# Kernel optimization log

Measured on AMD Instinct MI355X. Metric: run time of the kernel, lower is better.

Reference implementation:

```python
import jax, jax.numpy as jnp
import numpy as np

D_MODEL = 1024
HIDDEN = 4096
N_EXPERTS = 8
TOP_K = 2


def setup_inputs() -> dict:
    key = jax.random.key(0)
    ks = jax.random.split(key, 7)
    x = jax.random.normal(ks[0], (4, 2048, D_MODEL), dtype=jnp.float32)
    s = 0.02
    Wg = jax.random.normal(ks[1], (D_MODEL, N_EXPERTS), dtype=jnp.float32) * s
    bg = jnp.zeros((N_EXPERTS,), dtype=jnp.float32)
    W1 = jax.random.normal(ks[2], (N_EXPERTS, D_MODEL, HIDDEN), dtype=jnp.float32) * s
    b1 = jnp.zeros((N_EXPERTS, HIDDEN), dtype=jnp.float32)
    W2 = jax.random.normal(ks[3], (N_EXPERTS, HIDDEN, D_MODEL), dtype=jnp.float32) * s
    b2 = jnp.zeros((N_EXPERTS, D_MODEL), dtype=jnp.float32)
    return {"x": x, "Wg": Wg, "bg": bg, "W1": W1, "b1": b1, "W2": W2, "b2": b2}


def reference(x, Wg, bg, W1, b1, W2, b2):
    B, T, D = x.shape
    xf = x.reshape(-1, D)                      # (N, D)
    N = xf.shape[0]

    # --- top-k gate ---
    logits = xf @ Wg + bg                      # (N, E)
    all_probs = jax.nn.softmax(logits, axis=-1)
    topk_logits, topk_idx = jax.lax.top_k(logits, TOP_K)   # (N, k)
    topk_gates = jax.nn.softmax(topk_logits, axis=-1)      # (N, k), sums to 1

    # scatter gates into dense (N, E) masks (matches torch scatter_add_)
    rows = jnp.arange(N)[:, None]
    gate_mask = jnp.zeros((N, N_EXPERTS), dtype=xf.dtype).at[rows, topk_idx].add(topk_gates)
    dispatch_mask = jnp.zeros((N, N_EXPERTS), dtype=xf.dtype).at[rows, topk_idx].add(1.0)

    # --- experts: dense batched form; unselected tokens have gate 0 so math matches ---
    h = jnp.einsum('nd,edh->neh', xf, W1) + b1             # (N, E, H)
    h = jax.nn.relu(h)
    y = jnp.einsum('neh,ehd->ned', h, W2) + b2             # (N, E, D)
    out = jnp.einsum('ned,ne->nd', y, gate_mask)           # weighted combine
    outputs = out.reshape(B, T, D)

    # --- load-balance loss + metadata ---
    tokens_per_expert = (dispatch_mask > 0).sum(axis=0)
    assignment_fraction = gate_mask.sum(axis=0) / N
    expected_prob = all_probs.mean(axis=0)
    load_balance_loss = (expected_prob * assignment_fraction).sum() * N_EXPERTS

    return (outputs, load_balance_loss, tokens_per_expert, expected_prob, assignment_fraction)
```

## Files before the change

kernel.cpp:

```cpp
#include <hip/hip_runtime.h>
#include <stdint.h>

#define D_MODEL 1024
#define HID     4096
#define NE      8
#define NTOK    8192
#define NSLOT   (NTOK*2)
#define TM      128
#define MAX_RB  136
#define MPAD    (MAX_RB*TM)
#define HHALF   2048
#define GATE_BLOCKS 32

typedef unsigned short u16;
typedef __attribute__((ext_vector_type(8))) __bf16 bf16x8;
typedef __attribute__((ext_vector_type(4))) float  f32x4;

__device__ __forceinline__ u16 f2bu(float f){
  uint32_t u = __builtin_bit_cast(uint32_t, f);
  uint32_t r = (u + 0x7FFFu + ((u >> 16) & 1u)) >> 16;
  return (u16)r;
}

__device__ __forceinline__ void gload16(const u16* src, u16* lds){
  __builtin_amdgcn_global_load_lds((const __attribute__((address_space(1))) void*)src,
                                   (__attribute__((address_space(3))) void*)lds, 16, 0, 0);
}

__device__ __forceinline__ int xcd_swz(int w, int nwg){
  int q = nwg >> 3;
  return (w & 7) * q + (w >> 3);
}

#define WAITV(n) do{ asm volatile("s_waitcnt vmcnt(" #n ")" ::: "memory"); \
                     __builtin_amdgcn_sched_barrier(0); }while(0)
#define BARX()   do{ __builtin_amdgcn_sched_barrier(0); \
                     __builtin_amdgcn_s_barrier(); \
                     __builtin_amdgcn_sched_barrier(0); }while(0)

__global__ __launch_bounds__(256) void xcvt_kernel(const float* __restrict__ x, u16* __restrict__ x16){
  size_t i = (size_t)blockIdx.x*256 + threadIdx.x;
  const float4* p = (const float4*)(x + i*8);
  float4 a = p[0], b = p[1];
  u16 o[8] = {f2bu(a.x),f2bu(a.y),f2bu(a.z),f2bu(a.w),f2bu(b.x),f2bu(b.y),f2bu(b.z),f2bu(b.w)};
  *(int4*)(x16 + i*8) = *(int4*)o;
}

__global__ __launch_bounds__(256) void transpose_cvt(const float* __restrict__ in,
                                                     u16* __restrict__ out, int R, int C)
{
  __shared__ float tile[32][33];
  int e = blockIdx.z;
  int r0 = blockIdx.y * 32, c0 = blockIdx.x * 32;
  const float* src = in + (size_t)e * R * C;
  u16* dst = out + (size_t)e * R * C;
  int tx = threadIdx.x, ty = threadIdx.y;
#pragma unroll
  for (int i = 0; i < 4; i++){
    int r = r0 + ty + i*8;
    tile[ty + i*8][tx] = src[(size_t)r * C + c0 + tx];
  }
  __syncthreads();
#pragma unroll
  for (int i = 0; i < 4; i++){
    int c = c0 + ty + i*8;
    dst[(size_t)c * R + r0 + tx] = f2bu(tile[tx][ty + i*8]);
  }
}

__global__ __launch_bounds__(256) void gate_kernel(
    const float* __restrict__ x, const float* __restrict__ Wg, const float* __restrict__ bg,
    int* __restrict__ topk, float* __restrict__ gates,
    float* __restrict__ part_probs, float* __restrict__ part_assign, int* __restrict__ part_cnt)
{
  __shared__ float sp[256][8];
  __shared__ float sa[256][8];
  __shared__ int   sc[256][8];
  int t = threadIdx.x;
  int n = blockIdx.x * 256 + t;
  float lg[8];
#pragma unroll
  for (int e = 0; e < 8; e++) lg[e] = bg[e];
  const float4* xr = (const float4*)(x + (size_t)n * D_MODEL);
  for (int j = 0; j < D_MODEL/4; j++){
    float4 v = xr[j];
    const float* wr = Wg + (size_t)j * 32;
#pragma unroll
    for (int e = 0; e < 8; e++)
      lg[e] += v.x*wr[e] + v.y*wr[8+e] + v.z*wr[16+e] + v.w*wr[24+e];
  }
  float m = lg[0];
#pragma unroll
  for (int e = 1; e < 8; e++) m = fmaxf(m, lg[e]);
  float p[8]; float s = 0.f;
#pragma unroll
  for (int e = 0; e < 8; e++){ p[e] = expf(lg[e]-m); s += p[e]; }
  float inv = 1.f / s;
  int bi = 0; float best = lg[0];
#pragma unroll
  for (int e = 1; e < 8; e++) if (lg[e] > best){ best = lg[e]; bi = e; }
  int bi2 = 0; float best2 = -3.0e38f;
#pragma unroll
  for (int e = 0; e < 8; e++) if (e != bi && lg[e] > best2){ best2 = lg[e]; bi2 = e; }
  float t1 = expf(best2 - best);
  float g0 = 1.f / (1.f + t1);
  float g1 = t1 / (1.f + t1);
  topk[2*n] = bi;  topk[2*n+1] = bi2;
  gates[2*n] = g0; gates[2*n+1] = g1;
#pragma unroll
  for (int e = 0; e < 8; e++){
    sp[t][e] = p[e] * inv;
    sa[t][e] = (e == bi) ? g0 : ((e == bi2) ? g1 : 0.f);
    sc[t][e] = (e == bi || e == bi2) ? 1 : 0;
  }
  __syncthreads();
  if (t < 8){
    float s2 = 0.f; for (int i = 0; i < 256; i++) s2 += sp[i][t];
    part_probs[blockIdx.x*8 + t] = s2;
  } else if (t < 16){
    int e = t - 8; float s2 = 0.f; for (int i = 0; i < 256; i++) s2 += sa[i][e];
    part_assign[blockIdx.x*8 + e] = s2;
  } else if (t < 24){
    int e = t - 16; int c = 0; for (int i = 0; i < 256; i++) c += sc[i][e];
    part_cnt[blockIdx.x*8 + e] = c;
  }
}

__global__ __launch_bounds__(256) void scan_kernel(const int* __restrict__ part_cnt,
                                                   int* __restrict__ counts,
                                                   int* __restrict__ padded_off,
                                                   int* __restrict__ cursor,
                                                   int* __restrict__ block_expert,
                                                   int* __restrict__ routed)
{
  __shared__ int off[NE+1];
  int t = threadIdx.x;
  if (t == 0){
    int o = 0; off[0] = 0;
    for (int e = 0; e < NE; e++){
      int c = 0;
      for (int b = 0; b < GATE_BLOCKS; b++) c += part_cnt[b*8 + e];
      counts[e] = c;
      o += ((c + TM - 1) / TM) * TM;
      off[e+1] = o;
    }
    for (int e = 0; e <= NE; e++) padded_off[e] = off[e];
  }
  __syncthreads();
  if (t < NE) cursor[t] = 0;
  for (int rb = t; rb < MAX_RB; rb += 256){
    int e = -1;
    int r = rb * TM;
    for (int j = 0; j < NE; j++)
      if (r >= off[j] && r < off[j+1]) e = j;
    block_expert[rb] = e;
  }
  for (int i = t; i < MPAD; i += 256) routed[i] = -1;
}

__global__ __launch_bounds__(256) void place_kernel(const int* __restrict__ topk,
                                                    const int* __restrict__ padded_off,
                                                    int* __restrict__ cursor,
                                                    int* __restrict__ routed)
{
  int s = blockIdx.x * 256 + threadIdx.x;
  int e = topk[s];
  int pos = padded_off[e] + atomicAdd(&cursor[e], 1);
  routed[pos] = s;
}

__global__ __launch_bounds__(256, 3) void gemm1_kernel(
    const u16* __restrict__ x16, const u16* __restrict__ w1t, const float* __restrict__ b1,
    const int* __restrict__ routed, const int* __restrict__ block_expert,
    u16* __restrict__ h, int half)
{
  int l = xcd_swz(blockIdx.x, gridDim.x);
  int rb = l >> 4, cb = l & 15;
  int e = block_expert[rb];
  if (e < 0) return;
  __shared__ __align__(16) u16 Al[3][128][32];
  __shared__ __align__(16) u16 Bl[3][128][32];
  u16* AF = &Al[0][0][0];
  u16* BF = &Bl[0][0][0];
  int t = threadIdx.x;
  int lane = t & 63, wid = t >> 6;

  int srow0 = wid*32 + (lane >> 2);
  int sch = ((lane & 3) ^ ((lane >> 3) & 3)) * 8;

  int slot0 = routed[rb*TM + srow0];
  int slot1 = routed[rb*TM + srow0 + 16];
  int tok0 = slot0 >= 0 ? (slot0 >> 1) : 0;
  int tok1 = slot1 >= 0 ? (slot1 >> 1) : 0;
  const u16* srcA0 = x16 + (size_t)tok0 * D_MODEL + sch;
  const u16* srcA1 = x16 + (size_t)tok1 * D_MODEL + sch;
  const u16* wb = w1t + ((size_t)e*HID + (size_t)half*HHALF + (size_t)cb*128) * D_MODEL + sch;
  const u16* srcB0 = wb + (size_t)srow0 * D_MODEL;
  const u16* srcB1 = wb + (size_t)(srow0 + 16) * D_MODEL;

  int wr = wid >> 1, wc = wid & 1;
  int fr = lane & 15, fk = lane >> 4;
  int fkx8 = (fk ^ ((fr >> 1) & 3)) * 8;
  f32x4 acc[4][4];
#pragma unroll
  for (int i = 0; i < 4; i++)
#pragma unroll
    for (int j = 0; j < 4; j++) acc[i][j] = (f32x4){0.f,0.f,0.f,0.f};

#define STG1(bo, kk) do{ \
    gload16(srcA0 + (kk), AF + (bo) + wid*1024); \
    gload16(srcA1 + (kk), AF + (bo) + wid*1024 + 512); \
    gload16(srcB0 + (kk), BF + (bo) + wid*1024); \
    gload16(srcB1 + (kk), BF + (bo) + wid*1024 + 512); } while(0)

#define CMP1(bo) do{ \
    bf16x8 af[4], bf[4]; \
    _Pragma("unroll") \
    for (int mm = 0; mm < 4; mm++) af[mm] = *(const bf16x8*)(AF + (bo) + (wr*64 + mm*16 + fr)*32 + fkx8); \
    _Pragma("unroll") \
    for (int nn = 0; nn < 4; nn++) bf[nn] = *(const bf16x8*)(BF + (bo) + (wc*64 + nn*16 + fr)*32 + fkx8); \
    _Pragma("unroll") \
    for (int mm = 0; mm < 4; mm++) \
      _Pragma("unroll") \
      for (int nn = 0; nn < 4; nn++) \
        acc[mm][nn] = __builtin_amdgcn_mfma_f32_16x16x32_bf16(af[mm], bf[nn], acc[mm][nn], 0, 0, 0); } while(0)

  const int nk = D_MODEL/32;
  STG1(0, 0); STG1(4096, 32); STG1(8192, 64);
  int bo = 0;
  for (int i = 0; i < nk - 2; i++){
    WAITV(8);
    BARX();
    CMP1(bo);
    BARX();
    if (i < nk - 3) STG1(bo, (i+3)*32);
    bo = (bo == 8192) ? 0 : bo + 4096;
  }
  WAITV(4); BARX(); CMP1(bo); BARX();
  bo = (bo == 8192) ? 0 : bo + 4096;
  WAITV(0); BARX(); CMP1(bo);

  int r4 = fk * 4;
#pragma unroll
  for (int nn = 0; nn < 4; nn++){
    int ct = wc*64 + nn*16 + fr;
    float bias = b1[(size_t)e*HID + (size_t)half*HHALF + cb*128 + ct];
#pragma unroll
    for (int mm = 0; mm < 4; mm++){
#pragma unroll
      for (int r = 0; r < 4; r++){
        int rt = wr*64 + mm*16 + r4 + r;
        float v = acc[mm][nn][r] + bias;
        v = v > 0.f ? v : 0.f;
        h[(size_t)(rb*TM + rt) * HHALF + cb*128 + ct] = f2bu(v);
      }
    }
  }
#undef STG1
#undef CMP1
}

__global__ __launch_bounds__(256, 3) void gemm2_kernel(
    const u16* __restrict__ h, const u16* __restrict__ w2t,
    const int* __restrict__ routed, const int* __restrict__ block_expert,
    const float* __restrict__ gates, float* __restrict__ y, int half)
{
  int l = xcd_swz(blockIdx.x, gridDim.x);
  int rb = l >> 3, cb = l & 7;
  int e = block_expert[rb];
  if (e < 0) return;
  __shared__ __align__(16) u16 Al[3][128][32];
  __shared__ __align__(16) u16 Bl[3][128][32];
  __shared__ int   rslot[128];
  __shared__ float rgate[128];
  u16* AF = &Al[0][0][0];
  u16* BF = &Bl[0][0][0];
  int t = threadIdx.x;
  int lane = t & 63, wid = t >> 6;
  if (t < 128){
    int s = routed[rb*TM + t];
    rslot[t] = s;
    rgate[t] = (s >= 0) ? gates[s] : 0.f;
  }

  int srow0 = wid*32 + (lane >> 2);
  int sch = ((lane & 3) ^ ((lane >> 3) & 3)) * 8;
  const u16* srcA0 = h + (size_t)(rb*TM + srow0) * HHALF + sch;
  const u16* srcA1 = h + (size_t)(rb*TM + srow0 + 16) * HHALF + sch;
  const u16* wb = w2t + ((size_t)e*D_MODEL + (size_t)cb*128) * HID + (size_t)half*HHALF + sch;
  const u16* srcB0 = wb + (size_t)srow0 * HID;
  const u16* srcB1 = wb + (size_t)(srow0 + 16) * HID;

  int wr = wid >> 1, wc = wid & 1;
  int fr = lane & 15, fk = lane >> 4;
  int fkx8 = (fk ^ ((fr >> 1) & 3)) * 8;
  f32x4 acc[4][4];
#pragma unroll
  for (int i = 0; i < 4; i++)
#pragma unroll
    for (int j = 0; j < 4; j++) acc[i][j] = (f32x4){0.f,0.f,0.f,0.f};

#define STG2(bo, kk) do{ \
    gload16(srcA0 + (kk), AF + (bo) + wid*1024); \
    gload16(srcA1 + (kk), AF + (bo) + wid*1024 + 512); \
    gload16(srcB0 + (kk), BF + (bo) + wid*1024); \
    gload16(srcB1 + (kk), BF + (bo) + wid*1024 + 512); } while(0)

#define CMP2(bo) do{ \
    bf16x8 af[4], bf[4]; \
    _Pragma("unroll") \
    for (int mm = 0; mm < 4; mm++) af[mm] = *(const bf16x8*)(AF + (bo) + (wr*64 + mm*16 + fr)*32 + fkx8); \
    _Pragma("unroll") \
    for (int nn = 0; nn < 4; nn++) bf[nn] = *(const bf16x8*)(BF + (bo) + (wc*64 + nn*16 + fr)*32 + fkx8); \
    _Pragma("unroll") \
    for (int mm = 0; mm < 4; mm++) \
      _Pragma("unroll") \
      for (int nn = 0; nn < 4; nn++) \
        acc[mm][nn] = __builtin_amdgcn_mfma_f32_16x16x32_bf16(af[mm], bf[nn], acc[mm][nn], 0, 0, 0); } while(0)

  const int nk = HHALF/32;
  STG2(0, 0); STG2(4096, 32); STG2(8192, 64);
  int bo = 0;
  for (int i = 0; i < nk - 2; i++){
    WAITV(8);
    BARX();
    CMP2(bo);
    BARX();
    if (i < nk - 3) STG2(bo, (i+3)*32);
    bo = (bo == 8192) ? 0 : bo + 4096;
  }
  WAITV(4); BARX(); CMP2(bo); BARX();
  bo = (bo == 8192) ? 0 : bo + 4096;
  WAITV(0); BARX(); CMP2(bo);

  int r4 = fk * 4;
#pragma unroll
  for (int mm = 0; mm < 4; mm++){
#pragma unroll
    for (int r = 0; r < 4; r++){
      int rt = wr*64 + mm*16 + r4 + r;
      int slot = rslot[rt];
      if (slot < 0) continue;
      float g = rgate[rt];
#pragma unroll
      for (int nn = 0; nn < 4; nn++){
        int ct = wc*64 + nn*16 + fr;
        size_t idx = (size_t)slot * D_MODEL + cb*128 + ct;
        float val = g * acc[mm][nn][r];
        if (half == 0) y[idx] = val;
        else           y[idx] += val;
      }
    }
  }
#undef STG2
#undef CMP2
}

__global__ __launch_bounds__(256) void combine_kernel(
    const float* __restrict__ y, const int* __restrict__ topk, const float* __restrict__ gates,
    const float* __restrict__ b2, float* __restrict__ out)
{
  int i = blockIdx.x * 256 + threadIdx.x;
  int n = i >> 8;
  int d = (i & 255) * 4;
  float4 a  = *(const float4*)(y + (size_t)(2*n)   * D_MODEL + d);
  float4 b  = *(const float4*)(y + (size_t)(2*n+1) * D_MODEL + d);
  int e0 = topk[2*n], e1 = topk[2*n+1];
  float g0 = gates[2*n], g1 = gates[2*n+1];
  float4 c0 = *(const float4*)(b2 + (size_t)e0 * D_MODEL + d);
  float4 c1 = *(const float4*)(b2 + (size_t)e1 * D_MODEL + d);
  float4 o;
  o.x = a.x + b.x + g0*c0.x + g1*c1.x;
  o.y = a.y + b.y + g0*c0.y + g1*c1.y;
  o.z = a.z + b.z + g0*c0.z + g1*c1.z;
  o.w = a.w + b.w + g0*c0.w + g1*c1.w;
  *(float4*)(out + (size_t)n * D_MODEL + d) = o;
}

__global__ void finalize_kernel(const float* __restrict__ part_probs,
                                const float* __restrict__ part_assign,
                                const int* __restrict__ counts,
                                float* __restrict__ out_tail)
{
  __shared__ float ep[8], af[8];
  int t = threadIdx.x;
  if (t < 8){
    float s = 0.f;
    for (int b = 0; b < GATE_BLOCKS; b++) s += part_probs[b*8 + t];
    ep[t] = s / (float)NTOK;
  } else if (t < 16){
    int e = t - 8; float s = 0.f;
    for (int b = 0; b < GATE_BLOCKS; b++) s += part_assign[b*8 + e];
    af[e] = s / (float)NTOK;
  }
  __syncthreads();
  if (t == 0){
    float loss = 0.f;
    for (int e = 0; e < 8; e++) loss += ep[e] * af[e];
    out_tail[0] = loss * (float)NE;
  }
  if (t < 8){
    out_tail[1 + t]  = (float)counts[t];
    out_tail[9 + t]  = ep[t];
    out_tail[17 + t] = af[t];
  }
}

extern "C" void kernel_launch(void* const* d_in, const int* in_sizes, int n_in,
                              void* d_out, int out_size, void* d_ws, size_t ws_size,
                              hipStream_t stream)
{
  const float* x  = (const float*)d_in[0];
  const float* Wg = (const float*)d_in[1];
  const float* bg = (const float*)d_in[2];
  const float* W1 = (const float*)d_in[3];
  const float* b1 = (const float*)d_in[4];
  const float* W2 = (const float*)d_in[5];
  const float* b2 = (const float*)d_in[6];
  float* out = (float*)d_out;

  char* ws = (char*)d_ws;
  size_t o = 0;
  auto alloc = [&](size_t bytes) -> char* {
    char* p = ws + o; o = (o + bytes + 255) & ~(size_t)255; return p;
  };
  int*   topk        = (int*)   alloc((size_t)NSLOT*4);
  float* gates       = (float*) alloc((size_t)NSLOT*4);
  int*   counts      = (int*)   alloc(NE*4);
  int*   padded_off  = (int*)   alloc((NE+1)*4);
  int*   cursor      = (int*)   alloc(NE*4);
  int*   block_exp   = (int*)   alloc(MAX_RB*4);
  int*   routed      = (int*)   alloc((size_t)MPAD*4);
  float* part_probs  = (float*) alloc(GATE_BLOCKS*8*4);
  float* part_assign = (float*) alloc(GATE_BLOCKS*8*4);
  int*   part_cnt    = (int*)   alloc(GATE_BLOCKS*8*4);
  u16*   x16         = (u16*)   alloc((size_t)NTOK*D_MODEL*2);
  u16*   w1t         = (u16*)   alloc((size_t)NE*HID*D_MODEL*2);
  u16*   w2t         = (u16*)   alloc((size_t)NE*HID*D_MODEL*2);
  u16*   hbuf        = (u16*)   alloc((size_t)MPAD*HHALF*2);
  float* ybuf        = (float*) alloc((size_t)NSLOT*D_MODEL*4);
  (void)ws_size; (void)in_sizes; (void)n_in; (void)out_size;

  transpose_cvt<<<dim3(HID/32, D_MODEL/32, NE), dim3(32,8), 0, stream>>>(W1, w1t, D_MODEL, HID);
  transpose_cvt<<<dim3(D_MODEL/32, HID/32, NE), dim3(32,8), 0, stream>>>(W2, w2t, HID, D_MODEL);
  xcvt_kernel<<<(NTOK*D_MODEL)/(256*8), 256, 0, stream>>>(x, x16);
  gate_kernel<<<GATE_BLOCKS, 256, 0, stream>>>(x, Wg, bg, topk, gates, part_probs, part_assign, part_cnt);
  scan_kernel<<<1, 256, 0, stream>>>(part_cnt, counts, padded_off, cursor, block_exp, routed);
  place_kernel<<<NSLOT/256, 256, 0, stream>>>(topk, padded_off, cursor, routed);
  for (int half = 0; half < 2; half++){
    gemm1_kernel<<<16*MAX_RB, 256, 0, stream>>>(x16, w1t, b1, routed, block_exp, hbuf, half);
    gemm2_kernel<<<8*MAX_RB, 256, 0, stream>>>(hbuf, w2t, routed, block_exp, gates, ybuf, half);
  }
  combine_kernel<<<NTOK, 256, 0, stream>>>(ybuf, topk, gates, b2, out);
  finalize_kernel<<<1, 64, 0, stream>>>(part_probs, part_assign, counts, out + (size_t)NTOK*D_MODEL);
}
```

Before: 677.9 us.

## Fuse x bf16 conversion into gate kernel and drop hidden-dim split in expert GEMMs

The bf16 conversion of x now happens inside the gate kernel, which already streams x, so one launch and one full read of x are removed. The expert GEMMs no longer split the hidden dimension into two halves. gemm1 writes the full hidden activation and gemm2 reduces over all of it in one pass, which removes the read-modify-write accumulation of the fp32 y buffer and two kernel launches. In exchange, the hidden buffer doubles in size and the low-parallelism gate kernel takes on extra store traffic.

```diff
diff --git a/kernel.cpp b/kernel.cpp
--- a/kernel.cpp
+++ b/kernel.cpp
@@ -9,7 +9,6 @@
 #define TM      128
 #define MAX_RB  136
 #define MPAD    (MAX_RB*TM)
-#define HHALF   2048
 #define GATE_BLOCKS 32
 
 typedef unsigned short u16;
@@ -37,14 +36,6 @@
 #define BARX()   do{ __builtin_amdgcn_sched_barrier(0); \
                      __builtin_amdgcn_s_barrier(); \
                      __builtin_amdgcn_sched_barrier(0); }while(0)
-
-__global__ __launch_bounds__(256) void xcvt_kernel(const float* __restrict__ x, u16* __restrict__ x16){
-  size_t i = (size_t)blockIdx.x*256 + threadIdx.x;
-  const float4* p = (const float4*)(x + i*8);
-  float4 a = p[0], b = p[1];
-  u16 o[8] = {f2bu(a.x),f2bu(a.y),f2bu(a.z),f2bu(a.w),f2bu(b.x),f2bu(b.y),f2bu(b.z),f2bu(b.w)};
-  *(int4*)(x16 + i*8) = *(int4*)o;
-}
 
 __global__ __launch_bounds__(256) void transpose_cvt(const float* __restrict__ in,
                                                      u16* __restrict__ out, int R, int C)
@@ -70,7 +61,7 @@
 
 __global__ __launch_bounds__(256) void gate_kernel(
     const float* __restrict__ x, const float* __restrict__ Wg, const float* __restrict__ bg,
-    int* __restrict__ topk, float* __restrict__ gates,
+    int* __restrict__ topk, float* __restrict__ gates, u16* __restrict__ x16,
     float* __restrict__ part_probs, float* __restrict__ part_assign, int* __restrict__ part_cnt)
 {
   __shared__ float sp[256][8];
@@ -82,12 +73,17 @@
 #pragma unroll
   for (int e = 0; e < 8; e++) lg[e] = bg[e];
   const float4* xr = (const float4*)(x + (size_t)n * D_MODEL);
+  u16* xo = x16 + (size_t)n * D_MODEL;
+  u16 tmp[8];
   for (int j = 0; j < D_MODEL/4; j++){
     float4 v = xr[j];
     const float* wr = Wg + (size_t)j * 32;
 #pragma unroll
     for (int e = 0; e < 8; e++)
       lg[e] += v.x*wr[e] + v.y*wr[8+e] + v.z*wr[16+e] + v.w*wr[24+e];
+    int o4 = (j & 1) * 4;
+    tmp[o4+0] = f2bu(v.x); tmp[o4+1] = f2bu(v.y); tmp[o4+2] = f2bu(v.z); tmp[o4+3] = f2bu(v.w);
+    if (j & 1) *(int4*)(xo + (j-1)*4) = *(int4*)tmp;
   }
   float m = lg[0];
 #pragma unroll
@@ -169,13 +165,14 @@
   routed[pos] = s;
 }
 
+
 __global__ __launch_bounds__(256, 3) void gemm1_kernel(
     const u16* __restrict__ x16, const u16* __restrict__ w1t, const float* __restrict__ b1,
     const int* __restrict__ routed, const int* __restrict__ block_expert,
-    u16* __restrict__ h, int half)
+    u16* __restrict__ h)
 {
   int l = xcd_swz(blockIdx.x, gridDim.x);
-  int rb = l >> 4, cb = l & 15;
+  int rb = l >> 5, cb = l & 31;
   int e = block_expert[rb];
   if (e < 0) return;
   __shared__ __align__(16) u16 Al[3][128][32];
@@ -194,7 +191,7 @@
   int tok1 = slot1 >= 0 ? (slot1 >> 1) : 0;
   const u16* srcA0 = x16 + (size_t)tok0 * D_MODEL + sch;
   const u16* srcA1 = x16 + (size_t)tok1 * D_MODEL + sch;
-  const u16* wb = w1t + ((size_t)e*HID + (size_t)half*HHALF + (size_t)cb*128) * D_MODEL + sch;
+  const u16* wb = w1t + ((size_t)e*HID + (size_t)cb*128) * D_MODEL + sch;
   const u16* srcB0 = wb + (size_t)srow0 * D_MODEL;
   const u16* srcB1 = wb + (size_t)(srow0 + 16) * D_MODEL;
 
@@ -244,7 +241,7 @@
 #pragma unroll
   for (int nn = 0; nn < 4; nn++){
     int ct = wc*64 + nn*16 + fr;
-    float bias = b1[(size_t)e*HID + (size_t)half*HHALF + cb*128 + ct];
+    float bias = b1[(size_t)e*HID + cb*128 + ct];
 #pragma unroll
     for (int mm = 0; mm < 4; mm++){
 #pragma unroll
@@ -252,7 +249,7 @@
         int rt = wr*64 + mm*16 + r4 + r;
         float v = acc[mm][nn][r] + bias;
         v = v > 0.f ? v : 0.f;
-        h[(size_t)(rb*TM + rt) * HHALF + cb*128 + ct] = f2bu(v);
+        h[(size_t)(rb*TM + rt) * HID + cb*128 + ct] = f2bu(v);
       }
     }
   }
@@ -263,7 +260,7 @@
 __global__ __launch_bounds__(256, 3) void gemm2_kernel(
     const u16* __restrict__ h, const u16* __restrict__ w2t,
     const int* __restrict__ routed, const int* __restrict__ block_expert,
-    const float* __restrict__ gates, float* __restrict__ y, int half)
+    const float* __restrict__ gates, float* __restrict__ y)
 {
   int l = xcd_swz(blockIdx.x, gridDim.x);
   int rb = l >> 3, cb = l & 7;
@@ -285,9 +282,9 @@
 
   int srow0 = wid*32 + (lane >> 2);
   int sch = ((lane & 3) ^ ((lane >> 3) & 3)) * 8;
-  const u16* srcA0 = h + (size_t)(rb*TM + srow0) * HHALF + sch;
-  const u16* srcA1 = h + (size_t)(rb*TM + srow0 + 16) * HHALF + sch;
-  const u16* wb = w2t + ((size_t)e*D_MODEL + (size_t)cb*128) * HID + (size_t)half*HHALF + sch;
+  const u16* srcA0 = h + (size_t)(rb*TM + srow0) * HID + sch;
+  const u16* srcA1 = h + (size_t)(rb*TM + srow0 + 16) * HID + sch;
+  const u16* wb = w2t + ((size_t)e*D_MODEL + (size_t)cb*128) * HID + sch;
   const u16* srcB0 = wb + (size_t)srow0 * HID;
   const u16* srcB1 = wb + (size_t)(srow0 + 16) * HID;
 
@@ -318,7 +315,7 @@
       for (int nn = 0; nn < 4; nn++) \
         acc[mm][nn] = __builtin_amdgcn_mfma_f32_16x16x32_bf16(af[mm], bf[nn], acc[mm][nn], 0, 0, 0); } while(0)
 
-  const int nk = HHALF/32;
+  const int nk = HID/32;
   STG2(0, 0); STG2(4096, 32); STG2(8192, 64);
   int bo = 0;
   for (int i = 0; i < nk - 2; i++){
@@ -345,10 +342,7 @@
 #pragma unroll
       for (int nn = 0; nn < 4; nn++){
         int ct = wc*64 + nn*16 + fr;
-        size_t idx = (size_t)slot * D_MODEL + cb*128 + ct;
-        float val = g * acc[mm][nn][r];
-        if (half == 0) y[idx] = val;
-        else           y[idx] += val;
+        y[(size_t)slot * D_MODEL + cb*128 + ct] = g * acc[mm][nn][r];
       }
     }
   }
@@ -437,20 +431,17 @@
   u16*   x16         = (u16*)   alloc((size_t)NTOK*D_MODEL*2);
   u16*   w1t         = (u16*)   alloc((size_t)NE*HID*D_MODEL*2);
   u16*   w2t         = (u16*)   alloc((size_t)NE*HID*D_MODEL*2);
-  u16*   hbuf        = (u16*)   alloc((size_t)MPAD*HHALF*2);
+  u16*   hbuf        = (u16*)   alloc((size_t)MPAD*HID*2);
   float* ybuf        = (float*) alloc((size_t)NSLOT*D_MODEL*4);
   (void)ws_size; (void)in_sizes; (void)n_in; (void)out_size;
 
   transpose_cvt<<<dim3(HID/32, D_MODEL/32, NE), dim3(32,8), 0, stream>>>(W1, w1t, D_MODEL, HID);
   transpose_cvt<<<dim3(D_MODEL/32, HID/32, NE), dim3(32,8), 0, stream>>>(W2, w2t, HID, D_MODEL);
-  xcvt_kernel<<<(NTOK*D_MODEL)/(256*8), 256, 0, stream>>>(x, x16);
-  gate_kernel<<<GATE_BLOCKS, 256, 0, stream>>>(x, Wg, bg, topk, gates, part_probs, part_assign, part_cnt);
+  gate_kernel<<<GATE_BLOCKS, 256, 0, stream>>>(x, Wg, bg, topk, gates, x16, part_probs, part_assign, part_cnt);
   scan_kernel<<<1, 256, 0, stream>>>(part_cnt, counts, padded_off, cursor, block_exp, routed);
   place_kernel<<<NSLOT/256, 256, 0, stream>>>(topk, padded_off, cursor, routed);
-  for (int half = 0; half < 2; half++){
-    gemm1_kernel<<<16*MAX_RB, 256, 0, stream>>>(x16, w1t, b1, routed, block_exp, hbuf, half);
-    gemm2_kernel<<<8*MAX_RB, 256, 0, stream>>>(hbuf, w2t, routed, block_exp, gates, ybuf, half);
-  }
+  gemm1_kernel<<<32*MAX_RB, 256, 0, stream>>>(x16, w1t, b1, routed, block_exp, hbuf);
+  gemm2_kernel<<<8*MAX_RB, 256, 0, stream>>>(hbuf, w2t, routed, block_exp, gates, ybuf);
   combine_kernel<<<NTOK, 256, 0, stream>>>(ybuf, topk, gates, b2, out);
   finalize_kernel<<<1, 64, 0, stream>>>(part_probs, part_assign, counts, out + (size_t)NTOK*D_MODEL);
 }
```

New measurement: 695.2 us. +2.5%, slower.
